# Performance work log

Measured on AMD Instinct MI355X. Metric: run time of the kernel, lower is better.

Reference implementation:

```python
import jax, jax.numpy as jnp
import numpy as np

N = 4096      # 2 ** var_num, var_num = 12
L = 50        # trajectory length
A_NUM = 4     # number of action variables (len(id2actvar))


def setup_inputs() -> dict:
    key = jax.random.key(0)
    ks = jax.random.split(key, 6)
    scale = 0.5 / np.sqrt(N)  # keep recurrence spectrally stable over L steps
    return {
        "init_states": jax.random.normal(ks[0], (N,), dtype=jnp.float32),
        "trajectories": jax.random.uniform(ks[1], (L, A_NUM), dtype=jnp.float32),
        "T_base": jax.random.normal(ks[2], (N, N), dtype=jnp.float32) * scale,
        "A_mats": jax.random.normal(ks[3], (A_NUM, N, N), dtype=jnp.float32) * (scale / A_NUM),
        "b": jax.random.normal(ks[4], (N,), dtype=jnp.float32) * 0.1,
        "r": jax.random.normal(ks[5], (N,), dtype=jnp.float32),
    }


def reference(init_states, trajectories, T_base, A_mats, b, r):
    # init_states is read from x in the original model but never used in the loop.
    n = T_base.shape[0]
    interface0 = jnp.zeros((n,), dtype=T_base.dtype)  # tf.zeros(2**var_num)

    def step(old_interface, act):
        # action-conditioned circuit filter: T_t = T_base + sum_a act[a] * A_mats[a]
        T = T_base + jnp.einsum('a,anm->nm', act, A_mats)
        new_interface = T @ old_interface + b          # [N]
        exp_reward = jnp.sum(r * new_interface)        # tf.reduce_sum(exp_reward)
        return new_interface, exp_reward

    _, exp_rewards = jax.lax.scan(step, interface0, trajectories)
    return exp_rewards  # [L]
```

## Files before the change

kernel.cpp:

```cpp
#include <hip/hip_runtime.h>
#include <hip/hip_fp16.h>

#define NDIM   4096
#define LSTEPS 50
#define ANUM   4
#define NN     ((size_t)NDIM * (size_t)NDIM)
#define CHUNK1 25
#define CHUNK2 24

typedef unsigned int nuint4 __attribute__((ext_vector_type(4)));
typedef float        nfloat4 __attribute__((ext_vector_type(4)));

__global__ void init_kernel(const float* __restrict__ b, float* __restrict__ x1) {
    const int tid = threadIdx.x;
    const float4* bv = (const float4*)b;
    float4* xv = (float4*)x1;
#pragma unroll
    for (int i = 0; i < 4; i++) xv[tid + 256 * i] = bv[tid + 256 * i];
}

__global__ __launch_bounds__(256) void combine_kernel(
        const float* __restrict__ Tb, const float* __restrict__ Am,
        const float* __restrict__ traj, uint4* __restrict__ outbuf,
        int t0, int C) {
    __shared__ float sact[CHUNK1 * ANUM];
    const int tid = threadIdx.x;
    if (tid < C * ANUM)
        sact[tid] = traj[(size_t)(t0 + tid / ANUM) * ANUM + (tid % ANUM)];
    __syncthreads();

    const size_t gtid = (size_t)blockIdx.x * 256 + tid;
    const size_t e4   = gtid * 2;
    const float4* tb4 = (const float4*)Tb;
    const float4* am4 = (const float4*)Am;
    const size_t m4 = NN / 4;

    union F8 { float4 f4[2]; float f[8]; };
    F8 tb, am[4];
    tb.f4[0] = tb4[e4]; tb.f4[1] = tb4[e4 + 1];
#pragma unroll
    for (int m = 0; m < 4; m++) {
        am[m].f4[0] = am4[(size_t)m * m4 + e4];
        am[m].f4[1] = am4[(size_t)m * m4 + e4 + 1];
    }

    const size_t matq = NN / 8;
    for (int t = 0; t < C; t++) {
        const float w0 = sact[t * 4 + 0], w1 = sact[t * 4 + 1],
                    w2 = sact[t * 4 + 2], w3 = sact[t * 4 + 3];
        union { uint4 v; __half h[8]; } pk;
#pragma unroll
        for (int j = 0; j < 8; j++) {
            float v = tb.f[j];
            v = fmaf(w0, am[0].f[j], v);
            v = fmaf(w1, am[1].f[j], v);
            v = fmaf(w2, am[2].f[j], v);
            v = fmaf(w3, am[3].f[j], v);
            pk.h[j] = __float2half(v);
        }
        outbuf[(size_t)t * matq + gtid] = pk.v;
    }
}

__global__ __launch_bounds__(256) void step_kernel(
        const uint4* __restrict__ Tt,
        const float* __restrict__ x_in,
        float*       __restrict__ x_out,
        const float* __restrict__ b,
        const float* __restrict__ r,
        float*       __restrict__ out, int t) {
    const int tid  = threadIdx.x;
    const int wave = tid >> 6, lane = tid & 63;

    if (blockIdx.x == gridDim.x - 1) {
        __shared__ float parts[4];
        float s = 0.f;
#pragma unroll
        for (int i = 0; i < 16; i++) {
            const int idx = tid + 256 * i;
            s = fmaf(r[idx], x_in[idx], s);
        }
#pragma unroll
        for (int off = 32; off > 0; off >>= 1) s += __shfl_xor(s, off, 64);
        if (lane == 0) parts[wave] = s;
        __syncthreads();
        if (tid == 0) out[t - 1] = parts[0] + parts[1] + parts[2] + parts[3];
        return;
    }

    const int row = blockIdx.x * 4 + wave;
    const size_t rowq = (size_t)row * (NDIM / 8);
    const nuint4* Tn = (const nuint4*)Tt;
    const float4* xv = (const float4*)x_in;

    float acc = 0.f;
#pragma unroll
    for (int c = 0; c < 8; c++) {
        const int ci = c * 64 + lane;
        const nuint4 tv = __builtin_nontemporal_load(&Tn[rowq + ci]);
        const float4 xa = xv[ci * 2];
        const float4 xb = xv[ci * 2 + 1];
        union { nuint4 v; __half2 h2[4]; } u; u.v = tv;
        const float2 p0 = __half22float2(u.h2[0]);
        const float2 p1 = __half22float2(u.h2[1]);
        const float2 p2 = __half22float2(u.h2[2]);
        const float2 p3 = __half22float2(u.h2[3]);
        acc = fmaf(p0.x, xa.x, acc); acc = fmaf(p0.y, xa.y, acc);
        acc = fmaf(p1.x, xa.z, acc); acc = fmaf(p1.y, xa.w, acc);
        acc = fmaf(p2.x, xb.x, acc); acc = fmaf(p2.y, xb.y, acc);
        acc = fmaf(p3.x, xb.z, acc); acc = fmaf(p3.y, xb.w, acc);
    }
#pragma unroll
    for (int off = 32; off > 0; off >>= 1) acc += __shfl_xor(acc, off, 64);
    if (lane == 0) x_out[row] = acc + b[row];
}

__global__ void dot_kernel(const float* __restrict__ x, const float* __restrict__ r,
                           float* __restrict__ out_elem) {
    const int tid = threadIdx.x;
    const int wave = tid >> 6, lane = tid & 63;
    __shared__ float parts[4];
    float s = 0.f;
#pragma unroll
    for (int i = 0; i < 16; i++) {
        const int idx = tid + 256 * i;
        s = fmaf(r[idx], x[idx], s);
    }
#pragma unroll
    for (int off = 32; off > 0; off >>= 1) s += __shfl_xor(s, off, 64);
    if (lane == 0) parts[wave] = s;
    __syncthreads();
    if (tid == 0) *out_elem = parts[0] + parts[1] + parts[2] + parts[3];
}

__global__ __launch_bounds__(256) void step_f32_kernel(
        const float* __restrict__ Tb, const float* __restrict__ Am,
        const float* __restrict__ x_in, float* __restrict__ x_out,
        const float* __restrict__ b, const float* __restrict__ r,
        const float* __restrict__ traj, float* __restrict__ out, int t) {
    const int tid  = threadIdx.x;
    const int wave = tid >> 6, lane = tid & 63;

    if (blockIdx.x == gridDim.x - 1) {
        __shared__ float parts[4];
        float s = 0.f;
#pragma unroll
        for (int i = 0; i < 16; i++) {
            const int idx = tid + 256 * i;
            s = fmaf(r[idx], x_in[idx], s);
        }
#pragma unroll
        for (int off = 32; off > 0; off >>= 1) s += __shfl_xor(s, off, 64);
        if (lane == 0) parts[wave] = s;
        __syncthreads();
        if (tid == 0) out[t - 1] = parts[0] + parts[1] + parts[2] + parts[3];
        return;
    }

    const float a0 = traj[t * ANUM + 0], a1 = traj[t * ANUM + 1],
                a2 = traj[t * ANUM + 2], a3 = traj[t * ANUM + 3];
    const int row = blockIdx.x * 4 + wave;
    const nfloat4* mat[5] = {
        (const nfloat4*)Tb, (const nfloat4*)Am, (const nfloat4*)(Am + NN),
        (const nfloat4*)(Am + 2 * NN), (const nfloat4*)(Am + 3 * NN)};
    const size_t rowq = (size_t)row * (NDIM / 4);
    const float4* xv = (const float4*)x_in;

    float acc[5] = {0.f, 0.f, 0.f, 0.f, 0.f};
#pragma unroll
    for (int c = 0; c < 16; c++) {
        const int ci = c * 64 + lane;
        const float4 xa = xv[ci];
        const size_t qi = rowq + ci;
#pragma unroll
        for (int m = 0; m < 5; m++) {
            const nfloat4 v = __builtin_nontemporal_load(&mat[m][qi]);
            float a = acc[m];
            a = fmaf(v.x, xa.x, a); a = fmaf(v.y, xa.y, a);
            a = fmaf(v.z, xa.z, a); a = fmaf(v.w, xa.w, a);
            acc[m] = a;
        }
    }
    float s = acc[0] + a0 * acc[1] + a1 * acc[2] + a2 * acc[3] + a3 * acc[4];
#pragma unroll
    for (int off = 32; off > 0; off >>= 1) s += __shfl_xor(s, off, 64);
    if (lane == 0) x_out[row] = s + b[row];
}

extern "C" void kernel_launch(void* const* d_in, const int* in_sizes, int n_in,
                              void* d_out, int out_size, void* d_ws, size_t ws_size,
                              hipStream_t stream) {
    const float* traj = (const float*)d_in[1];
    const float* Tb   = (const float*)d_in[2];
    const float* Am   = (const float*)d_in[3];
    const float* b    = (const float*)d_in[4];
    const float* r    = (const float*)d_in[5];
    float* out = (float*)d_out;

    const size_t chunkBytes = (size_t)CHUNK1 * NN * sizeof(__half);
    const size_t xBytes     = 2 * (size_t)NDIM * sizeof(float);
    const bool useChunks = ws_size >= chunkBytes + xBytes;

    if (useChunks) {
        uint4* chunk = (uint4*)d_ws;
        float* x0 = (float*)((char*)d_ws + chunkBytes);
        float* x1 = x0 + NDIM;
        const size_t matq = NN / 8;
        const int combBlocks = (int)(matq / 256);

        init_kernel<<<1, 256, 0, stream>>>(b, x0);

        combine_kernel<<<combBlocks, 256, 0, stream>>>(Tb, Am, traj, chunk, 1, CHUNK1);
        for (int t = 1; t <= CHUNK1; t++) {
            float* xi = (t & 1) ? x0 : x1;
            float* xo = (t & 1) ? x1 : x0;
            step_kernel<<<NDIM / 4 + 1, 256, 0, stream>>>(
                chunk + (size_t)(t - 1) * matq, xi, xo, b, r, out, t);
        }
        combine_kernel<<<combBlocks, 256, 0, stream>>>(Tb, Am, traj, chunk,
                                                       CHUNK1 + 1, CHUNK2);
        for (int t = CHUNK1 + 1; t < LSTEPS; t++) {
            float* xi = (t & 1) ? x0 : x1;
            float* xo = (t & 1) ? x1 : x0;
            step_kernel<<<NDIM / 4 + 1, 256, 0, stream>>>(
                chunk + (size_t)(t - CHUNK1 - 1) * matq, xi, xo, b, r, out, t);
        }
        dot_kernel<<<1, 256, 0, stream>>>(x1, r, out + (LSTEPS - 1));
    } else {
        float* x0 = (float*)d_ws;
        float* x1 = x0 + NDIM;
        init_kernel<<<1, 256, 0, stream>>>(b, x0);
        for (int t = 1; t < LSTEPS; t++) {
            float* xi = (t & 1) ? x0 : x1;
            float* xo = (t & 1) ? x1 : x0;
            step_f32_kernel<<<NDIM / 4 + 1, 256, 0, stream>>>(Tb, Am, xi, xo, b, r,
                                                              traj, out, t);
        }
        dot_kernel<<<1, 256, 0, stream>>>(x1, r, out + (LSTEPS - 1));
    }
}
```

Measured before the change: 1.709 ms.

## Keep fp16 base and action matrices resident and combine per row in-kernel

Stops materialising a full fp16 transition matrix for every step. Instead, the base matrix and the four action matrices are converted once to fp16 in a row-interleaved layout. Each step kernel then computes five partial dot products per row and mixes them with that step's action weights. Non-temporal loads are dropped so the roughly 160MB working set can stay in the last-level cache across steps. The trade-off is that each step reads five times as many matrix bytes, so the change only pays off if the interleaved set stays cache-resident rather than streaming from HBM.

```diff
diff --git a/kernel.cpp b/kernel.cpp
--- a/kernel.cpp
+++ b/kernel.cpp
@@ -5,11 +5,10 @@
 #define LSTEPS 50
 #define ANUM   4
 #define NN     ((size_t)NDIM * (size_t)NDIM)
-#define CHUNK1 25
-#define CHUNK2 24
+#define ROWQ   512
+#define RSTRIDE (5 * ROWQ)
 
 typedef unsigned int nuint4 __attribute__((ext_vector_type(4)));
-typedef float        nfloat4 __attribute__((ext_vector_type(4)));
 
 __global__ void init_kernel(const float* __restrict__ b, float* __restrict__ x1) {
     const int tid = threadIdx.x;
@@ -19,61 +18,41 @@
     for (int i = 0; i < 4; i++) xv[tid + 256 * i] = bv[tid + 256 * i];
 }
 
-__global__ __launch_bounds__(256) void combine_kernel(
+__global__ __launch_bounds__(256) void conv_kernel(
         const float* __restrict__ Tb, const float* __restrict__ Am,
-        const float* __restrict__ traj, uint4* __restrict__ outbuf,
-        int t0, int C) {
-    __shared__ float sact[CHUNK1 * ANUM];
-    const int tid = threadIdx.x;
-    if (tid < C * ANUM)
-        sact[tid] = traj[(size_t)(t0 + tid / ANUM) * ANUM + (tid % ANUM)];
-    __syncthreads();
-
-    const size_t gtid = (size_t)blockIdx.x * 256 + tid;
-    const size_t e4   = gtid * 2;
-    const float4* tb4 = (const float4*)Tb;
-    const float4* am4 = (const float4*)Am;
-    const size_t m4 = NN / 4;
-
-    union F8 { float4 f4[2]; float f[8]; };
-    F8 tb, am[4];
-    tb.f4[0] = tb4[e4]; tb.f4[1] = tb4[e4 + 1];
-#pragma unroll
-    for (int m = 0; m < 4; m++) {
-        am[m].f4[0] = am4[(size_t)m * m4 + e4];
-        am[m].f4[1] = am4[(size_t)m * m4 + e4 + 1];
-    }
-
-    const size_t matq = NN / 8;
-    for (int t = 0; t < C; t++) {
-        const float w0 = sact[t * 4 + 0], w1 = sact[t * 4 + 1],
-                    w2 = sact[t * 4 + 2], w3 = sact[t * 4 + 3];
-        union { uint4 v; __half h[8]; } pk;
-#pragma unroll
-        for (int j = 0; j < 8; j++) {
-            float v = tb.f[j];
-            v = fmaf(w0, am[0].f[j], v);
-            v = fmaf(w1, am[1].f[j], v);
-            v = fmaf(w2, am[2].f[j], v);
-            v = fmaf(w3, am[3].f[j], v);
-            pk.h[j] = __float2half(v);
-        }
-        outbuf[(size_t)t * matq + gtid] = pk.v;
-    }
-}
-
-__global__ __launch_bounds__(256) void step_kernel(
-        const uint4* __restrict__ Tt,
+        uint4* __restrict__ dst) {
+    const size_t gid = (size_t)blockIdx.x * 256 + threadIdx.x;
+    const size_t perMat = NN / 8;
+    const int    m   = (int)(gid / perMat);
+    const size_t rem = gid - (size_t)m * perMat;
+    const int    rw  = (int)(rem >> 9);
+    const int    c   = (int)(rem & 511);
+
+    const float* src = (m == 0) ? Tb : (Am + (size_t)(m - 1) * NN);
+    const float4* s4 = (const float4*)src;
+    const float4 f0 = s4[rem * 2];
+    const float4 f1 = s4[rem * 2 + 1];
+    union { uint4 v; __half h[8]; } pk;
+    pk.h[0] = __float2half(f0.x); pk.h[1] = __float2half(f0.y);
+    pk.h[2] = __float2half(f0.z); pk.h[3] = __float2half(f0.w);
+    pk.h[4] = __float2half(f1.x); pk.h[5] = __float2half(f1.y);
+    pk.h[6] = __float2half(f1.z); pk.h[7] = __float2half(f1.w);
+    dst[(size_t)rw * RSTRIDE + (size_t)m * ROWQ + c] = pk.v;
+}
+
+__global__ __launch_bounds__(256, 4) void step5_kernel(
+        const nuint4* __restrict__ M,
         const float* __restrict__ x_in,
         float*       __restrict__ x_out,
         const float* __restrict__ b,
         const float* __restrict__ r,
+        const float* __restrict__ traj,
         float*       __restrict__ out, int t) {
     const int tid  = threadIdx.x;
     const int wave = tid >> 6, lane = tid & 63;
+    __shared__ float parts[4];
 
     if (blockIdx.x == gridDim.x - 1) {
-        __shared__ float parts[4];
         float s = 0.f;
 #pragma unroll
         for (int i = 0; i < 16; i++) {
@@ -89,30 +68,36 @@
     }
 
     const int row = blockIdx.x * 4 + wave;
-    const size_t rowq = (size_t)row * (NDIM / 8);
-    const nuint4* Tn = (const nuint4*)Tt;
+    const size_t base = (size_t)row * RSTRIDE;
     const float4* xv = (const float4*)x_in;
-
-    float acc = 0.f;
+    const float4 av = ((const float4*)traj)[t];
+
+    float acc[5] = {0.f, 0.f, 0.f, 0.f, 0.f};
 #pragma unroll
     for (int c = 0; c < 8; c++) {
         const int ci = c * 64 + lane;
-        const nuint4 tv = __builtin_nontemporal_load(&Tn[rowq + ci]);
         const float4 xa = xv[ci * 2];
         const float4 xb = xv[ci * 2 + 1];
-        union { nuint4 v; __half2 h2[4]; } u; u.v = tv;
-        const float2 p0 = __half22float2(u.h2[0]);
-        const float2 p1 = __half22float2(u.h2[1]);
-        const float2 p2 = __half22float2(u.h2[2]);
-        const float2 p3 = __half22float2(u.h2[3]);
-        acc = fmaf(p0.x, xa.x, acc); acc = fmaf(p0.y, xa.y, acc);
-        acc = fmaf(p1.x, xa.z, acc); acc = fmaf(p1.y, xa.w, acc);
-        acc = fmaf(p2.x, xb.x, acc); acc = fmaf(p2.y, xb.y, acc);
-        acc = fmaf(p3.x, xb.z, acc); acc = fmaf(p3.y, xb.w, acc);
-    }
-#pragma unroll
-    for (int off = 32; off > 0; off >>= 1) acc += __shfl_xor(acc, off, 64);
-    if (lane == 0) x_out[row] = acc + b[row];
+#pragma unroll
+        for (int m = 0; m < 5; m++) {
+            union { nuint4 v; __half2 h2[4]; } u;
+            u.v = M[base + (size_t)m * ROWQ + ci];
+            const float2 p0 = __half22float2(u.h2[0]);
+            const float2 p1 = __half22float2(u.h2[1]);
+            const float2 p2 = __half22float2(u.h2[2]);
+            const float2 p3 = __half22float2(u.h2[3]);
+            float a = acc[m];
+            a = fmaf(p0.x, xa.x, a); a = fmaf(p0.y, xa.y, a);
+            a = fmaf(p1.x, xa.z, a); a = fmaf(p1.y, xa.w, a);
+            a = fmaf(p2.x, xb.x, a); a = fmaf(p2.y, xb.y, a);
+            a = fmaf(p3.x, xb.z, a); a = fmaf(p3.y, xb.w, a);
+            acc[m] = a;
+        }
+    }
+    float s = acc[0] + av.x * acc[1] + av.y * acc[2] + av.z * acc[3] + av.w * acc[4];
+#pragma unroll
+    for (int off = 32; off > 0; off >>= 1) s += __shfl_xor(s, off, 64);
+    if (lane == 0) x_out[row] = s + b[row];
 }
 
 __global__ void dot_kernel(const float* __restrict__ x, const float* __restrict__ r,
@@ -140,9 +125,9 @@
         const float* __restrict__ traj, float* __restrict__ out, int t) {
     const int tid  = threadIdx.x;
     const int wave = tid >> 6, lane = tid & 63;
+    __shared__ float parts[4];
 
     if (blockIdx.x == gridDim.x - 1) {
-        __shared__ float parts[4];
         float s = 0.f;
 #pragma unroll
         for (int i = 0; i < 16; i++) {
@@ -160,9 +145,9 @@
     const float a0 = traj[t * ANUM + 0], a1 = traj[t * ANUM + 1],
                 a2 = traj[t * ANUM + 2], a3 = traj[t * ANUM + 3];
     const int row = blockIdx.x * 4 + wave;
-    const nfloat4* mat[5] = {
-        (const nfloat4*)Tb, (const nfloat4*)Am, (const nfloat4*)(Am + NN),
-        (const nfloat4*)(Am + 2 * NN), (const nfloat4*)(Am + 3 * NN)};
+    const float4* mat[5] = {
+        (const float4*)Tb, (const float4*)Am, (const float4*)(Am + NN),
+        (const float4*)(Am + 2 * NN), (const float4*)(Am + 3 * NN)};
     const size_t rowq = (size_t)row * (NDIM / 4);
     const float4* xv = (const float4*)x_in;
 
@@ -174,7 +159,7 @@
         const size_t qi = rowq + ci;
 #pragma unroll
         for (int m = 0; m < 5; m++) {
-            const nfloat4 v = __builtin_nontemporal_load(&mat[m][qi]);
+            const float4 v = mat[m][qi];
             float a = acc[m];
             a = fmaf(v.x, xa.x, a); a = fmaf(v.y, xa.y, a);
             a = fmaf(v.z, xa.z, a); a = fmaf(v.w, xa.w, a);
@@ -197,33 +182,24 @@
     const float* r    = (const float*)d_in[5];
     float* out = (float*)d_out;
 
-    const size_t chunkBytes = (size_t)CHUNK1 * NN * sizeof(__half);
-    const size_t xBytes     = 2 * (size_t)NDIM * sizeof(float);
-    const bool useChunks = ws_size >= chunkBytes + xBytes;
-
-    if (useChunks) {
-        uint4* chunk = (uint4*)d_ws;
-        float* x0 = (float*)((char*)d_ws + chunkBytes);
+    const size_t matBytes = 5 * NN * sizeof(__half);
+    const size_t xBytes   = 2 * (size_t)NDIM * sizeof(float);
+    const bool useHalf = ws_size >= matBytes + xBytes;
+
+    if (useHalf) {
+        uint4* mats = (uint4*)d_ws;
+        float* x0 = (float*)((char*)d_ws + matBytes);
         float* x1 = x0 + NDIM;
-        const size_t matq = NN / 8;
-        const int combBlocks = (int)(matq / 256);
 
         init_kernel<<<1, 256, 0, stream>>>(b, x0);
-
-        combine_kernel<<<combBlocks, 256, 0, stream>>>(Tb, Am, traj, chunk, 1, CHUNK1);
-        for (int t = 1; t <= CHUNK1; t++) {
+        const int convBlocks = (int)((5 * NN / 8) / 256);
+        conv_kernel<<<convBlocks, 256, 0, stream>>>(Tb, Am, mats);
+
+        for (int t = 1; t < LSTEPS; t++) {
             float* xi = (t & 1) ? x0 : x1;
             float* xo = (t & 1) ? x1 : x0;
-            step_kernel<<<NDIM / 4 + 1, 256, 0, stream>>>(
-                chunk + (size_t)(t - 1) * matq, xi, xo, b, r, out, t);
-        }
-        combine_kernel<<<combBlocks, 256, 0, stream>>>(Tb, Am, traj, chunk,
-                                                       CHUNK1 + 1, CHUNK2);
-        for (int t = CHUNK1 + 1; t < LSTEPS; t++) {
-            float* xi = (t & 1) ? x0 : x1;
-            float* xo = (t & 1) ? x1 : x0;
-            step_kernel<<<NDIM / 4 + 1, 256, 0, stream>>>(
-                chunk + (size_t)(t - CHUNK1 - 1) * matq, xi, xo, b, r, out, t);
+            step5_kernel<<<NDIM / 4 + 1, 256, 0, stream>>>(
+                (const nuint4*)mats, xi, xo, b, r, traj, out, t);
         }
         dot_kernel<<<1, 256, 0, stream>>>(x1, r, out + (LSTEPS - 1));
     } else {
```

New measurement: 1.603 ms. 1.07x faster.
